# Optimization experiments

Hardware: AMD Instinct MI355X
Metric: run time of the kernel (lower is better)

## Reference

```python
import jax, jax.numpy as jnp
import numpy as np

B, NQ, NK, D_IN, D_H = 2, 8192, 8192, 256, 256


def setup_inputs() -> dict:
    key = jax.random.key(0)
    ks = jax.random.split(key, 9)
    s = 1.0 / np.sqrt(D_IN)
    return {
        "q": jax.random.normal(ks[0], (B, NQ, D_IN), jnp.float32),
        "k": jax.random.normal(ks[1], (B, NK, D_IN), jnp.float32),
        "v": jax.random.normal(ks[2], (B, NK, D_IN), jnp.float32),
        "Wq": jax.random.uniform(ks[3], (D_IN, D_H), jnp.float32, -s, s),
        "bq": jax.random.uniform(ks[4], (D_H,), jnp.float32, -s, s),
        "Wk": jax.random.uniform(ks[5], (D_IN, D_H), jnp.float32, -s, s),
        "bk": jax.random.uniform(ks[6], (D_H,), jnp.float32, -s, s),
        "Wv": jax.random.uniform(ks[7], (D_IN, D_H), jnp.float32, -s, s),
        "bv": jax.random.uniform(ks[8], (D_H,), jnp.float32, -s, s),
        "chunk_size": 1024,
    }


def reference(q, k, v, Wq, bq, Wk, bk, Wv, bv, chunk_size):
    # Projections (nn.Linear: x @ W + b)
    q_emb = q @ Wq + bq            # [B, NQ, D_H]
    k_emb = k @ Wk + bk            # [B, NK, D_H]
    v_emb = v @ Wv + bv            # value_emb=True -> project v
    # NOTE: original applies NO 1/sqrt(d) scaling.
    # Query chunking in the original is a pure memory optimization;
    # softmax is over the full key axis, so full attention is identical math.
    scores = jnp.einsum("bqd,bkd->bqk", q_emb, k_emb)  # [B, NQ, NK]
    probs = jax.nn.softmax(scores, axis=-1)
    out = jnp.einsum("bqk,bkd->bqd", probs, v_emb)     # [B, NQ, D_H]
    return out
```

## Files before the change

kernel.cpp:

```cpp
#include <hip/hip_runtime.h>

#define B_   2
#define NQ_  8192
#define NK_  8192
#define DIN_ 256
#define DH_  256
#define M_   (B_ * NQ_)

typedef _Float16 f16x8 __attribute__((ext_vector_type(8)));
typedef unsigned short u16x8 __attribute__((ext_vector_type(8)));
typedef unsigned short u16x4 __attribute__((ext_vector_type(4)));
typedef unsigned int  u32x4 __attribute__((ext_vector_type(4)));
typedef float f32x16 __attribute__((ext_vector_type(16)));

__device__ __forceinline__ unsigned short f2h(float f) {
    _Float16 h = (_Float16)f;
    return __builtin_bit_cast(unsigned short, h);
}
__device__ __forceinline__ float h2f(unsigned short u) {
    return (float)__builtin_bit_cast(_Float16, u);
}

__global__ void wt_conv(const float* __restrict__ Wq, const float* __restrict__ Wk,
                        const float* __restrict__ Wv, unsigned short* __restrict__ wt) {
    __shared__ float tile[64][65];
    const int mat = blockIdx.z;
    const int k0 = blockIdx.x * 64, n0 = blockIdx.y * 64;
    const float* W = (mat == 0) ? Wq : (mat == 1) ? Wk : Wv;
#pragma unroll
    for (int p = 0; p < 16; ++p) {
        const int idx = p * 256 + threadIdx.x;
        const int r = idx >> 6, c = idx & 63;
        tile[r][c] = W[(k0 + r) * 256 + n0 + c];
    }
    __syncthreads();
#pragma unroll
    for (int p = 0; p < 16; ++p) {
        const int idx = p * 256 + threadIdx.x;
        const int nr = idx >> 6, kc = idx & 63;
        wt[mat * 65536 + (n0 + nr) * 256 + k0 + kc] = f2h(tile[kc][nr]);
    }
}

__global__ __launch_bounds__(256) void proj(
    const float* __restrict__ xq, const float* __restrict__ xk, const float* __restrict__ xv,
    const float* __restrict__ bq, const float* __restrict__ bk, const float* __restrict__ bv,
    const unsigned short* __restrict__ wt,
    unsigned short* __restrict__ q_emb, unsigned short* __restrict__ k_emb,
    unsigned short* __restrict__ vpack) {
    const int mat = blockIdx.y;
    const float* x    = (mat == 0) ? xq : (mat == 1) ? xk : xv;
    const float* bias = (mat == 0) ? bq : (mat == 1) ? bk : bv;
    const unsigned short* w = wt + mat * 65536;

    const int tid = threadIdx.x;
    const int l = tid & 63, wv = tid >> 6;
    const int pair = wv >> 1, h = wv & 1;
    const int lm = l & 31, lh = l >> 5;
    const int row0 = blockIdx.x * 64;
    const int m = row0 + pair * 32 + lm;

    f32x16 acc[4];
#pragma unroll
    for (int i = 0; i < 4; ++i)
#pragma unroll
        for (int j = 0; j < 16; ++j) acc[i][j] = 0.0f;

#pragma unroll
    for (int ks = 0; ks < 16; ++ks) {
        const float4* ap = (const float4*)(x + (size_t)m * 256 + ks * 16 + lh * 8);
        float4 a0 = ap[0], a1 = ap[1];
        u16x8 au;
        au[0] = f2h(a0.x); au[1] = f2h(a0.y); au[2] = f2h(a0.z); au[3] = f2h(a0.w);
        au[4] = f2h(a1.x); au[5] = f2h(a1.y); au[6] = f2h(a1.z); au[7] = f2h(a1.w);
        f16x8 af = __builtin_bit_cast(f16x8, au);
#pragma unroll
        for (int nt = 0; nt < 4; ++nt) {
            f16x8 bfr = *(const f16x8*)(w + (h * 128 + nt * 32 + lm) * 256 + ks * 16 + lh * 8);
            acc[nt] = __builtin_amdgcn_mfma_f32_32x32x16_f16(af, bfr, acc[nt], 0, 0, 0);
        }
    }

    if (mat < 2) {
        unsigned short* emb = (mat == 0) ? q_emb : k_emb;
#pragma unroll
        for (int nt = 0; nt < 4; ++nt) {
            const int n = h * 128 + nt * 32 + lm;
            const float bsv = bias[n];
#pragma unroll
            for (int r = 0; r < 16; ++r) {
                const int rl = (r & 3) + 8 * (r >> 2) + 4 * lh;
                emb[(size_t)(row0 + pair * 32 + rl) * 256 + n] = f2h(acc[nt][r] + bsv);
            }
        }
    } else {
        const int batch = row0 >> 13;
        const int m0 = (row0 & 8191) + pair * 32;
        unsigned short* vp = vpack + (size_t)batch * (512 * 8 * 64 * 8);
        const int base_kt = m0 >> 4;
#pragma unroll
        for (int nt = 0; nt < 4; ++nt) {
            const int dg = h * 4 + nt;
            const int n = h * 128 + nt * 32 + lm;
            const float bsv = bias[n];
#pragma unroll
            for (int g = 0; g < 4; ++g) {
                u16x4 pk;
#pragma unroll
                for (int i = 0; i < 4; ++i) pk[i] = f2h(acc[nt][4 * g + i] + bsv);
                const int kt = base_kt + (g >> 1);
                const int lane = (g & 1) * 32 + lm;
                *(u16x4*)(vp + ((size_t)(kt * 8 + dg) * 64 + lane) * 8 + lh * 4) = pk;
            }
        }
    }
}

#define BN_ 128
#define NT_ (NK_ / BN_)
#define KB_BYTES 65536
#define PSTRIDE 272
#define PBYTES  (64 * PSTRIDE)
#define STAT_OFF (2 * KB_BYTES + PBYTES)
#define LDS_TOTAL (STAT_OFF + 2048)

__global__ __launch_bounds__(512, 2) void flash(
    const unsigned short* __restrict__ q_emb, const unsigned short* __restrict__ k_emb,
    const unsigned short* __restrict__ vpack, float* __restrict__ out) {
    __shared__ __align__(16) char lds_raw[LDS_TOTAL];
    char* pbuf = lds_raw + 2 * KB_BYTES;
    float* smax = (float*)(lds_raw + STAT_OFF);
    float* ssum = smax + 256;

    const int tid = threadIdx.x;
    const int l = tid & 63, wv = tid >> 6;
    const int kq = wv >> 1, pair = wv & 1;
    const int lm = l & 31, lh = l >> 5;

    const int bx = blockIdx.x;
    const int batch = bx >> 7;
    const int qb = (bx & 127) * 64;

    const unsigned short* kg = k_emb + (size_t)batch * NK_ * 256;
    const unsigned short* vp = vpack + (size_t)batch * (512 * 8 * 64 * 8);

    const int mrow = batch * NQ_ + qb + pair * 32 + lm;
    f16x8 qf[16];
#pragma unroll
    for (int ks = 0; ks < 16; ++ks)
        qf[ks] = *(const f16x8*)(q_emb + (size_t)mrow * 256 + ks * 16 + lh * 8);

    f32x16 oacc[2];
#pragma unroll
    for (int i = 0; i < 2; ++i)
#pragma unroll
        for (int j = 0; j < 16; ++j) oacc[i][j] = 0.0f;

    float mstat = -3.0e38f, lstat = 0.0f;

    const int rlane = l >> 5;
    const int gl = l & 31;
    auto stage_k = [&](int kb, char* kdst) {
#pragma unroll
        for (int p = 0; p < 8; ++p) {
            const int r0 = wv * 16 + 2 * p;
            const int r = r0 + rlane;
            const int gsw = gl ^ (r & 31);
            const unsigned short* src = kg + (size_t)(kb + r) * 256 + gsw * 8;
            __builtin_amdgcn_global_load_lds(
                (const __attribute__((address_space(1))) void*)src,
                (__attribute__((address_space(3))) void*)(kdst + r0 * 512),
                16, 0, 0);
        }
    };

    f16x8 vf[16];
    auto load_v = [&](int kb) {
        const size_t kt0 = (size_t)(kb >> 4);
#pragma unroll
        for (int ks2 = 0; ks2 < 8; ++ks2)
#pragma unroll
            for (int dt = 0; dt < 2; ++dt)
                vf[ks2 * 2 + dt] = *(const f16x8*)(
                    vp + (((kt0 + ks2) * 8 + kq * 2 + dt) * 64 + l) * 8);
    };

    stage_k(0, lds_raw);
    __syncthreads();

    const int prow = pair * 32 + lm;

    for (int t = 0; t < NT_; ++t) {
        const int kb = t * BN_;
        char* kcur = lds_raw + (t & 1) * KB_BYTES;
        if (t + 1 < NT_) stage_k(kb + BN_, lds_raw + ((t + 1) & 1) * KB_BYTES);
        load_v(kb);

        f32x16 s;
#pragma unroll
        for (int j = 0; j < 16; ++j) s[j] = 0.0f;
#pragma unroll
        for (int ks = 0; ks < 16; ++ks) {
            const int gsw = (2 * ks + lh) ^ lm;
            f16x8 kf = *(const f16x8*)(kcur + (kq * 32 + lm) * 512 + gsw * 16);
            s = __builtin_amdgcn_mfma_f32_32x32x16_f16(kf, qf[ks], s, 0, 0, 0);
        }

        float pm = s[0];
#pragma unroll
        for (int j = 1; j < 16; ++j) pm = fmaxf(pm, s[j]);
        pm = fmaxf(pm, __shfl_xor(pm, 32, 64));
        if (lh == 0) smax[prow * 4 + kq] = pm;
        __syncthreads();

        const float4 m4 = *(const float4*)&smax[prow * 4];
        const float gm = fmaxf(fmaxf(m4.x, m4.y), fmaxf(m4.z, m4.w));
        const float mn = fmaxf(mstat, gm);
        const float alpha = __expf(mstat - mn);
        mstat = mn;

        float psum = 0.0f;
#pragma unroll
        for (int g = 0; g < 4; ++g) {
            u16x4 pk;
#pragma unroll
            for (int j = 0; j < 4; ++j) {
                const unsigned short hh = f2h(__expf(s[g * 4 + j] - mn));
                pk[j] = hh;
                psum += h2f(hh);
            }
            *(u16x4*)(pbuf + prow * PSTRIDE + (kq * 32 + 8 * g + 4 * lh) * 2) = pk;
        }
        psum += __shfl_xor(psum, 32, 64);
        if (lh == 0) ssum[prow * 4 + kq] = psum;
        __syncthreads();

        const float4 s4 = *(const float4*)&ssum[prow * 4];
        lstat = lstat * alpha + (s4.x + s4.y) + (s4.z + s4.w);

#pragma unroll
        for (int dt = 0; dt < 2; ++dt)
#pragma unroll
            for (int j = 0; j < 16; ++j) oacc[dt][j] *= alpha;

#pragma unroll
        for (int ks2 = 0; ks2 < 8; ++ks2) {
            f16x8 pf = *(const f16x8*)(pbuf + prow * PSTRIDE + ks2 * 32 + lh * 16);
#pragma unroll
            for (int dt = 0; dt < 2; ++dt)
                oacc[dt] = __builtin_amdgcn_mfma_f32_32x32x16_f16(vf[ks2 * 2 + dt], pf,
                                                                  oacc[dt], 0, 0, 0);
        }
    }

    const float linv = 1.0f / lstat;
    float* orow = out + (size_t)(batch * NQ_ + qb + pair * 32 + lm) * 256;
#pragma unroll
    for (int dt = 0; dt < 2; ++dt) {
#pragma unroll
        for (int g = 0; g < 4; ++g) {
            float4 o4;
            o4.x = oacc[dt][4 * g + 0] * linv;
            o4.y = oacc[dt][4 * g + 1] * linv;
            o4.z = oacc[dt][4 * g + 2] * linv;
            o4.w = oacc[dt][4 * g + 3] * linv;
            *(float4*)(orow + kq * 64 + dt * 32 + 8 * g + 4 * lh) = o4;
        }
    }
}

extern "C" void kernel_launch(void* const* d_in, const int* in_sizes, int n_in,
                              void* d_out, int out_size, void* d_ws, size_t ws_size,
                              hipStream_t stream) {
    const float* q  = (const float*)d_in[0];
    const float* k  = (const float*)d_in[1];
    const float* v  = (const float*)d_in[2];
    const float* Wq = (const float*)d_in[3];
    const float* bq = (const float*)d_in[4];
    const float* Wk = (const float*)d_in[5];
    const float* bk = (const float*)d_in[6];
    const float* Wv = (const float*)d_in[7];
    const float* bv = (const float*)d_in[8];
    float* out = (float*)d_out;

    unsigned short* wt      = (unsigned short*)d_ws;
    unsigned short* q_emb   = wt + 3 * 65536;
    unsigned short* k_emb   = q_emb + (size_t)M_ * DH_;
    unsigned short* vpack   = k_emb + (size_t)M_ * DH_;

    wt_conv<<<dim3(4, 4, 3), 256, 0, stream>>>(Wq, Wk, Wv, wt);
    proj<<<dim3(256, 3), 256, 0, stream>>>(q, k, v, bq, bk, bv, wt, q_emb, k_emb, vpack);
    flash<<<256, 512, 0, stream>>>(q_emb, k_emb, vpack, out);
}
```

Before: 328.6 us.

## Repartition PV MFMA so each wave owns one 32-column V tile across both query halves

The P·V stage is re-tiled so each of the 8 waves handles a single 32-wide slice of the output head dimension for all 64 query rows, instead of a 64-wide slice for 32 rows. This halves per-wave V register fragments and V global loads (8 instead of 16 f16x8 per tile), at the cost of reading two P rows from LDS per k-step. Per-row alpha and 1/l are shared through new LDS slots, with an extra barrier before the epilogue. The aim is lower register pressure and less redundant V traffic.

```diff
diff --git a/kernel.cpp b/kernel.cpp
--- a/kernel.cpp
+++ b/kernel.cpp
@@ -131,6 +131,8 @@
     char* pbuf = lds_raw + 2 * KB_BYTES;
     float* smax = (float*)(lds_raw + STAT_OFF);
     float* ssum = smax + 256;
+    float* alph = ssum + 256;
+    float* linvb = alph + 64;
 
     const int tid = threadIdx.x;
     const int l = tid & 63, wv = tid >> 6;
@@ -174,15 +176,12 @@
         }
     };
 
-    f16x8 vf[16];
+    f16x8 vf[8];
     auto load_v = [&](int kb) {
         const size_t kt0 = (size_t)(kb >> 4);
 #pragma unroll
         for (int ks2 = 0; ks2 < 8; ++ks2)
-#pragma unroll
-            for (int dt = 0; dt < 2; ++dt)
-                vf[ks2 * 2 + dt] = *(const f16x8*)(
-                    vp + (((kt0 + ks2) * 8 + kq * 2 + dt) * 64 + l) * 8);
+            vf[ks2] = *(const f16x8*)(vp + (((kt0 + ks2) * 8 + wv) * 64 + l) * 8);
     };
 
     stage_k(0, lds_raw);
@@ -218,6 +217,7 @@
         const float mn = fmaxf(mstat, gm);
         const float alpha = __expf(mstat - mn);
         mstat = mn;
+        if (kq == 0 && lh == 0) alph[prow] = alpha;
 
         float psum = 0.0f;
 #pragma unroll
@@ -238,33 +238,39 @@
         const float4 s4 = *(const float4*)&ssum[prow * 4];
         lstat = lstat * alpha + (s4.x + s4.y) + (s4.z + s4.w);
 
-#pragma unroll
-        for (int dt = 0; dt < 2; ++dt)
-#pragma unroll
-            for (int j = 0; j < 16; ++j) oacc[dt][j] *= alpha;
+        const float a0 = alph[lm];
+        const float a1 = alph[lm + 32];
+#pragma unroll
+        for (int j = 0; j < 16; ++j) oacc[0][j] *= a0;
+#pragma unroll
+        for (int j = 0; j < 16; ++j) oacc[1][j] *= a1;
 
 #pragma unroll
         for (int ks2 = 0; ks2 < 8; ++ks2) {
-            f16x8 pf = *(const f16x8*)(pbuf + prow * PSTRIDE + ks2 * 32 + lh * 16);
-#pragma unroll
-            for (int dt = 0; dt < 2; ++dt)
-                oacc[dt] = __builtin_amdgcn_mfma_f32_32x32x16_f16(vf[ks2 * 2 + dt], pf,
-                                                                  oacc[dt], 0, 0, 0);
-        }
-    }
-
-    const float linv = 1.0f / lstat;
-    float* orow = out + (size_t)(batch * NQ_ + qb + pair * 32 + lm) * 256;
-#pragma unroll
-    for (int dt = 0; dt < 2; ++dt) {
+            const f16x8 vfr = vf[ks2];
+            f16x8 pf0 = *(const f16x8*)(pbuf + lm * PSTRIDE + ks2 * 32 + lh * 16);
+            f16x8 pf1 = *(const f16x8*)(pbuf + (lm + 32) * PSTRIDE + ks2 * 32 + lh * 16);
+            oacc[0] = __builtin_amdgcn_mfma_f32_32x32x16_f16(vfr, pf0, oacc[0], 0, 0, 0);
+            oacc[1] = __builtin_amdgcn_mfma_f32_32x32x16_f16(vfr, pf1, oacc[1], 0, 0, 0);
+        }
+    }
+
+    if (kq == 0 && lh == 0) linvb[prow] = 1.0f / lstat;
+    __syncthreads();
+    const float linv0 = linvb[lm];
+    const float linv1 = linvb[lm + 32];
+#pragma unroll
+    for (int qt = 0; qt < 2; ++qt) {
+        const float lv = qt ? linv1 : linv0;
+        float* orow = out + (size_t)(batch * NQ_ + qb + qt * 32 + lm) * 256 + wv * 32;
 #pragma unroll
         for (int g = 0; g < 4; ++g) {
             float4 o4;
-            o4.x = oacc[dt][4 * g + 0] * linv;
-            o4.y = oacc[dt][4 * g + 1] * linv;
-            o4.z = oacc[dt][4 * g + 2] * linv;
-            o4.w = oacc[dt][4 * g + 3] * linv;
-            *(float4*)(orow + kq * 64 + dt * 32 + 8 * g + 4 * lh) = o4;
+            o4.x = oacc[qt][4 * g + 0] * lv;
+            o4.y = oacc[qt][4 * g + 1] * lv;
+            o4.z = oacc[qt][4 * g + 2] * lv;
+            o4.w = oacc[qt][4 * g + 3] * lv;
+            *(float4*)(orow + 8 * g + 4 * lh) = o4;
         }
     }
 }
```

After: 314.7 us. 1.04x faster.
